# Kernel tuning notes

Hardware: AMD Instinct MI355X
Metric: run time of the kernel (lower is better)

## Reference

```python
import jax, jax.numpy as jnp
import numpy as np

B, IN_SEQ, TGT_SEQ = 128, 50, 25
IN_SIZE, OUT_SIZE, RNN = 128, 128, 2048


def setup_inputs() -> dict:
    key = jax.random.key(0)
    ks = jax.random.split(key, 10)
    s_in = 1.0 / np.sqrt(IN_SIZE)
    s_out = 1.0 / np.sqrt(OUT_SIZE)
    s_rnn = 1.0 / np.sqrt(RNN)
    return {
        "encoder_inputs": jax.random.normal(ks[0], (B, IN_SEQ, IN_SIZE), jnp.float32),
        "decoder_inputs": jax.random.normal(ks[1], (B, TGT_SEQ, IN_SIZE), jnp.float32),
        "fc1_w": jax.random.uniform(ks[2], (OUT_SIZE, IN_SIZE), jnp.float32, -s_in, s_in),
        "fc1_b": jax.random.uniform(ks[3], (OUT_SIZE,), jnp.float32, -s_in, s_in),
        "w_ih": jax.random.uniform(ks[4], (3 * RNN, OUT_SIZE), jnp.float32, -s_rnn, s_rnn),
        "w_hh": jax.random.uniform(ks[5], (3 * RNN, RNN), jnp.float32, -s_rnn, s_rnn),
        "b_ih": jax.random.uniform(ks[6], (3 * RNN,), jnp.float32, -s_rnn, s_rnn),
        "b_hh": jax.random.uniform(ks[7], (3 * RNN,), jnp.float32, -s_rnn, s_rnn),
        "fc2_w": jax.random.uniform(ks[8], (OUT_SIZE, RNN), jnp.float32, -s_rnn, s_rnn),
        "fc2_b": jax.random.uniform(ks[9], (OUT_SIZE,), jnp.float32, -s_rnn, s_rnn),
    }


def _gru_cell(x, h, w_ih, w_hh, b_ih, b_hh):
    # PyTorch GRUCell: gates ordered (r, z, n)
    gi = x @ w_ih.T + b_ih            # [B, 3R]
    gh = h @ w_hh.T + b_hh            # [B, 3R]
    i_r, i_z, i_n = jnp.split(gi, 3, axis=-1)
    h_r, h_z, h_n = jnp.split(gh, 3, axis=-1)
    r = jax.nn.sigmoid(i_r + h_r)
    z = jax.nn.sigmoid(i_z + h_z)
    n = jnp.tanh(i_n + r * h_n)
    return (1.0 - z) * n + z * h


def reference(encoder_inputs, decoder_inputs, fc1_w, fc1_b, w_ih, w_hh, b_ih, b_hh, fc2_w, fc2_b):
    # Eval mode: F.dropout(training=False) is identity.
    enc = encoder_inputs @ fc1_w.T + fc1_b              # [B, S_in, OUT]
    enc_t = jnp.transpose(enc, (1, 0, 2))               # time-major [S_in, B, OUT]
    h0 = jnp.zeros((encoder_inputs.shape[0], RNN), enc.dtype)

    def enc_step(state, x):
        return _gru_cell(x, state, w_ih, w_hh, b_ih, b_hh), None

    state, _ = jax.lax.scan(enc_step, h0, enc_t[:-1])   # input_seq - 1 steps

    def dec_step(carry, _):
        state, inp = carry
        inp = jax.lax.stop_gradient(inp)                # inp.detach()
        state = _gru_cell(inp, state, w_ih, w_hh, b_ih, b_hh)
        out = inp + state @ fc2_w.T + fc2_b             # residual decoder
        return (state, out), out

    _, outs = jax.lax.scan(dec_step, (state, enc_t[-1]), None, length=TGT_SEQ)
    return jnp.transpose(outs, (1, 0, 2))               # [B, TGT_SEQ, OUT]
```

## Files before the change

kernel.cpp:

```cpp
#include <hip/hip_runtime.h>
#include <limits.h>

constexpr int kB   = 128;
constexpr int kSin = 50;
constexpr int kT   = 25;
constexpr int kD   = 128;
constexpr int kR   = 2048;
constexpr int kNB  = 256;
constexpr int kNT  = 512;

typedef __bf16 bf16x8 __attribute__((ext_vector_type(8)));
typedef float  f32x4  __attribute__((ext_vector_type(4)));
typedef unsigned short u16;
typedef unsigned long long u64;

__device__ __forceinline__ float bf2f(u16 u){ union{unsigned i; float f;}x; x.i=((unsigned)u)<<16; return x.f; }
__device__ __forceinline__ u16 f2bf(float f){ union{float f; unsigned i;}x; x.f=f; return (u16)((x.i + 0x7FFFu + ((x.i>>16)&1u))>>16); }
__device__ __forceinline__ float sigm(float x){ return 1.f/(1.f+__expf(-x)); }

__device__ __forceinline__ void stg32(unsigned* p, unsigned v){
    __hip_atomic_store(p, v, __ATOMIC_RELAXED, __HIP_MEMORY_SCOPE_AGENT);
}
__device__ __forceinline__ void stg64(u64* p, u64 v){
    __hip_atomic_store(p, v, __ATOMIC_RELAXED, __HIP_MEMORY_SCOPE_AGENT);
}

__device__ __forceinline__ bf16x8 pack8(float4 a, float4 b){
    union{ bf16x8 v; u16 u[8]; } t;
    t.u[0]=f2bf(a.x); t.u[1]=f2bf(a.y); t.u[2]=f2bf(a.z); t.u[3]=f2bf(a.w);
    t.u[4]=f2bf(b.x); t.u[5]=f2bf(b.y); t.u[6]=f2bf(b.z); t.u[7]=f2bf(b.w);
    return t.v;
}

__device__ __forceinline__ void gbar(int* flags, int* genp, int k)
{
    __syncthreads();
    if (threadIdx.x == 0) atomicMax(&flags[blockIdx.x], k);
    if (blockIdx.x == 0 && threadIdx.x < 64) {
        const int i0 = (int)threadIdx.x * 4;
        for (;;) {
            int a = atomicMax(&flags[i0+0], INT_MIN);
            int b = atomicMax(&flags[i0+1], INT_MIN);
            int c = atomicMax(&flags[i0+2], INT_MIN);
            int d = atomicMax(&flags[i0+3], INT_MIN);
            if (__ballot((a>=k)&&(b>=k)&&(c>=k)&&(d>=k)) == ~0ull) break;
            __builtin_amdgcn_s_sleep(2);
        }
        if (threadIdx.x == 0) atomicMax(genp, k);
    }
    if (threadIdx.x == 0) {
        while (atomicMax(genp, INT_MIN) < k) __builtin_amdgcn_s_sleep(2);
        __builtin_amdgcn_fence(__ATOMIC_ACQUIRE, "agent");
    }
    __syncthreads();
}

__device__ __forceinline__ void cvt_f32_bf16(const float* __restrict__ s, u16* __restrict__ d,
                                             int n4, int gtid, int gstride)
{
    for (int i = gtid; i < n4; i += gstride) {
        float4 v = ((const float4*)s)[i];
        u64 pk = (u64)f2bf(v.x) | ((u64)f2bf(v.y)<<16) | ((u64)f2bf(v.z)<<32) | ((u64)f2bf(v.w)<<48);
        stg64((u64*)d + i, pk);
    }
}

template<int NT, int NACC>
__device__ __forceinline__ void small_gemm(
    const u16* __restrict__ Am, int alda,
    const u16* __restrict__ Bp, int bldb,
    f32x4 (&acc)[NACC], u16* pool)
{
    const int tid=threadIdx.x, lane=tid&63, wv=tid>>6, g=wv>>2, mt=wv&3, ar=lane&15, aq=lane>>4;
    u16* sA = pool;
    u16* sB = pool + 8704;
    { int q=tid,     r=q>>4, c=q&15; *(uint4*)&sA[r*136+c*8] = *(const uint4*)(Am + r*alda + c*8); }
    { int q=tid+512, r=q>>4, c=q&15; *(uint4*)&sA[r*136+c*8] = *(const uint4*)(Am + r*alda + c*8); }
    for (int q=tid; q<NT*256; q+=kNT){
        int r=q>>4, c=q&15;
        *(uint4*)&sB[r*136+c*8] = *(const uint4*)(Bp + (size_t)r*bldb + c*8);
    }
    __syncthreads();
#pragma unroll
    for (int jt=0; jt<NT; ++jt){
        if ((jt&1) != g) continue;
#pragma unroll
        for (int kk=0; kk<4; ++kk){
            bf16x8 a = *(const bf16x8*)&sA[(mt*16+ar)*136 + kk*32 + aq*8];
            bf16x8 b = *(const bf16x8*)&sB[(jt*16+ar)*136 + kk*32 + aq*8];
            acc[jt>>1] = __builtin_amdgcn_mfma_f32_16x16x32_bf16(a,b,acc[jt>>1],0,0,0);
        }
    }
    __syncthreads();
}

__device__ __forceinline__ void gru_phase_reg(
    const u16* __restrict__ hcur, u16* __restrict__ hnxt,
    const u16* __restrict__ xb,
    const bf16x8 (&wB)[3][8], const bf16x8 (&wI)[3],
    const float* __restrict__ bias,
    int wgc, int mrow0, u16* smem)
{
    const int tid=threadIdx.x, lane=tid&63, w=tid>>6, ar=lane&15, aq=lane>>4;
    const f32x4 zz = {0.f,0.f,0.f,0.f};
    f32x4 acc[3][4] = {{zz,zz,zz,zz},{zz,zz,zz,zz},{zz,zz,zz,zz}};
    f32x4 xn[4] = {zz,zz,zz,zz};

#pragma unroll
    for (int mt=0; mt<4; ++mt){
        const int row = mrow0 + mt*16 + ar;
        bf16x8 af[8];
#pragma unroll
        for (int c=0; c<8; ++c){
            const int s = 16*w + 2*c + (aq>>1);
            af[c] = *(const bf16x8*)(hcur + (((s*128 + row)<<4) + (aq&1)*8));
        }
#pragma unroll
        for (int c=0; c<8; ++c){
            acc[0][mt] = __builtin_amdgcn_mfma_f32_16x16x32_bf16(af[c], wB[0][c], acc[0][mt],0,0,0);
            acc[1][mt] = __builtin_amdgcn_mfma_f32_16x16x32_bf16(af[c], wB[1][c], acc[1][mt],0,0,0);
            acc[2][mt] = __builtin_amdgcn_mfma_f32_16x16x32_bf16(af[c], wB[2][c], acc[2][mt],0,0,0);
        }
    }
    if (w < 4){
#pragma unroll
        for (int mt=0; mt<4; ++mt){
            bf16x8 ax = *(const bf16x8*)(xb + (mrow0+mt*16+ar)*kD + 32*w + aq*8);
            acc[0][mt] = __builtin_amdgcn_mfma_f32_16x16x32_bf16(ax, wI[0], acc[0][mt],0,0,0);
            acc[1][mt] = __builtin_amdgcn_mfma_f32_16x16x32_bf16(ax, wI[1], acc[1][mt],0,0,0);
            xn[mt]     = __builtin_amdgcn_mfma_f32_16x16x32_bf16(ax, wI[2], xn[mt],0,0,0);
        }
    }
    float* red = (float*)smem;
#define RCELL(wp,g4,mt) (red + (((((wp)*4+(g4))*4+(mt))*64 + lane)<<2))
    if (w >= 4){
#pragma unroll
        for (int g=0; g<3; ++g)
#pragma unroll
            for (int mt=0; mt<4; ++mt)
                *(f32x4*)RCELL(w-4, g, mt) = acc[g][mt];
    }
    __syncthreads();
    if (w < 4){
#pragma unroll
        for (int g=0; g<3; ++g)
#pragma unroll
            for (int mt=0; mt<4; ++mt)
                acc[g][mt] += *(f32x4*)RCELL(w, g, mt);
#pragma unroll
        for (int g=0; g<3; ++g)
#pragma unroll
            for (int mt=0; mt<4; ++mt)
                *(f32x4*)RCELL(w, g, mt) = acc[g][mt];
#pragma unroll
        for (int mt=0; mt<4; ++mt)
            *(f32x4*)RCELL(w, 3, mt) = xn[mt];
    }
    __syncthreads();
    if (tid < 256){
        const int mt = tid>>6, ls = tid&63, aqs = ls>>4, ars = ls&15;
        f32x4 R=zz, Z=zz, NH=zz, NX=zz;
#pragma unroll
        for (int wp=0; wp<4; ++wp){
            R  += *(f32x4*)(red + ((((wp*4+0)*4+mt)*64 + ls)<<2));
            Z  += *(f32x4*)(red + ((((wp*4+1)*4+mt)*64 + ls)<<2));
            NH += *(f32x4*)(red + ((((wp*4+2)*4+mt)*64 + ls)<<2));
            NX += *(f32x4*)(red + ((((wp*4+3)*4+mt)*64 + ls)<<2));
        }
        const int hc = wgc*16 + ars;
        const float brz = bias[hc]      + bias[3*kR+hc];
        const float bzz = bias[kR+hc]   + bias[4*kR+hc];
        const float bin = bias[2*kR+hc];
        const float bhn = bias[5*kR+hc];
#pragma unroll
        for (int rr=0; rr<4; ++rr){
            const int m = mrow0 + mt*16 + aqs*4 + rr;
            float r_ = sigm(R[rr] + brz);
            float z_ = sigm(Z[rr] + bzz);
            float n_ = tanhf(NX[rr] + bin + r_*(NH[rr] + bhn));
            float hp = bf2f(hcur[((wgc*128 + m)<<4) + ars]);
            u16 hb = f2bf((1.f-z_)*n_ + z_*hp);
            unsigned other = (unsigned)__shfl_xor((int)(unsigned)hb, 1);
            if (!(ars&1))
                stg32((unsigned*)(hnxt + ((wgc*128+m)<<4) + ars), (unsigned)hb | (other<<16));
        }
    }
#undef RCELL
    __syncthreads();
}

__device__ __forceinline__ void fc2_gemm(
    const u16* __restrict__ hnew, const u16* __restrict__ WF2,
    int mrow0, int nt, int ks, float* __restrict__ part_tile, u16* smem)
{
    const int tid=threadIdx.x, lane=tid&63, wv=tid>>6, ar=lane&15, aq=lane>>4;
    u16* sA = smem;
    u16* sB = smem + 8704;
#pragma unroll
    for (int rep=0; rep<2; ++rep){
        int q = tid + rep*512, r = q>>4, c = q&15;
        int s = ks*8 + (c>>1), off = (c&1)*8;
        *(uint4*)&sA[r*136+c*8] = *(const uint4*)(hnew + (((s*128 + mrow0 + r)<<4) + off));
    }
    if (tid < 256){
        int r = tid>>4, c = tid&15;
        *(uint4*)&sB[r*136+c*8] = *(const uint4*)(WF2 + (size_t)(nt*16+r)*kR + ks*128 + c*8);
    }
    __syncthreads();
    if (wv < 4){
        const int mt = wv;
        f32x4 ao = {0.f,0.f,0.f,0.f};
#pragma unroll
        for (int kk=0; kk<4; ++kk){
            bf16x8 a = *(const bf16x8*)&sA[(mt*16+ar)*136 + kk*32 + aq*8];
            bf16x8 b = *(const bf16x8*)&sB[ar*136 + kk*32 + aq*8];
            ao = __builtin_amdgcn_mfma_f32_16x16x32_bf16(a,b,ao,0,0,0);
        }
#pragma unroll
        for (int rr=0; rr<4; ++rr)
            stg32((unsigned*)(part_tile + (mt*16 + aq*4 + rr)*16 + ar), __float_as_uint(ao[rr]));
    }
    __syncthreads();
}

__global__ __launch_bounds__(kNT, 2) void seq2seq_kernel(
    const void* __restrict__ enc_in_raw, const void* __restrict__ fc1_w_raw,
    const void* __restrict__ fc1_b_raw,  const void* __restrict__ w_ih_raw,
    const void* __restrict__ w_hh_raw,   const void* __restrict__ b_ih_raw,
    const void* __restrict__ b_hh_raw,   const void* __restrict__ fc2_w_raw,
    const void* __restrict__ fc2_b_raw,
    void* __restrict__ out_raw,
    u16* __restrict__ enc_act,
    u16* __restrict__ h_b16,
    u16* __restrict__ inp_b16,
    float* __restrict__ inp_f32,
    float* __restrict__ encF,
    float* __restrict__ bias,
    float* __restrict__ part,
    int* flags, int* genp,
    u16* __restrict__ cv_encx, u16* __restrict__ cv_fc2, u16* __restrict__ cv_fc1)
{
    __shared__ __align__(16) u16 smem[32768];
    __shared__ int sflag;
    const int wg = blockIdx.x, tid = threadIdx.x;
    const int wgc = wg & 127, mrow0 = (wg >> 7) * 64;
    const int lane = tid & 63, wv = tid >> 6, ar = lane & 15, aq = lane >> 4;
    const int gtid = wg * kNT + tid, gstride = kNB * kNT;
    int tok = 1;

    {
        const u16* p = (const u16*)enc_in_raw;
        int found = 0;
        for (int i = tid; i < 16384; i += kNT) found |= ((p[i] & 0x7F80) == 0x7F80) ? 1 : 0;
        if (tid == 0) sflag = 0;
        __syncthreads();
        if (found) sflag = 1;
        __syncthreads();
    }
    const bool F32 = (sflag != 0);

    bf16x8 wB[3][8];
    bf16x8 wI[3];
    {
        const int w4 = wv & 3;
        if (F32){
            const float* Wh = (const float*)w_hh_raw;
            const float* Wi = (const float*)w_ih_raw;
#pragma unroll
            for (int g=0; g<3; ++g)
#pragma unroll
                for (int c=0; c<8; ++c){
                    size_t o = (size_t)(g*kR + wgc*16 + ar)*kR + 256*wv + 32*c + aq*8;
                    wB[g][c] = pack8(*(const float4*)(Wh+o), *(const float4*)(Wh+o+4));
                }
#pragma unroll
            for (int g=0; g<3; ++g){
                size_t o = (size_t)(g*kR + wgc*16 + ar)*kD + 32*w4 + aq*8;
                wI[g] = pack8(*(const float4*)(Wi+o), *(const float4*)(Wi+o+4));
            }
        } else {
            const u16* Wh = (const u16*)w_hh_raw;
            const u16* Wi = (const u16*)w_ih_raw;
#pragma unroll
            for (int g=0; g<3; ++g)
#pragma unroll
                for (int c=0; c<8; ++c)
                    wB[g][c] = *(const bf16x8*)(Wh + (size_t)(g*kR + wgc*16 + ar)*kR + 256*wv + 32*c + aq*8);
#pragma unroll
            for (int g=0; g<3; ++g)
                wI[g] = *(const bf16x8*)(Wi + (size_t)(g*kR + wgc*16 + ar)*kD + 32*w4 + aq*8);
        }
    }

    if (F32) {
        cvt_f32_bf16((const float*)fc2_w_raw, cv_fc2,  (kD*kR)/4,       gtid, gstride);
        cvt_f32_bf16((const float*)fc1_w_raw, cv_fc1,  (kD*kD)/4,       gtid, gstride);
        cvt_f32_bf16((const float*)enc_in_raw,cv_encx, (kB*kSin*kD)/4,  gtid, gstride);
        for (int i = gtid; i < 3*kR; i += gstride) {
            stg32((unsigned*)&bias[i],        __float_as_uint(((const float*)b_ih_raw)[i]));
            stg32((unsigned*)&bias[3*kR + i], __float_as_uint(((const float*)b_hh_raw)[i]));
        }
        for (int i = gtid; i < kD; i += gstride) {
            stg32((unsigned*)&bias[6*kR + i],      __float_as_uint(((const float*)fc1_b_raw)[i]));
            stg32((unsigned*)&bias[6*kR + kD + i], __float_as_uint(((const float*)fc2_b_raw)[i]));
        }
    } else {
        for (int i = gtid; i < 3*kR; i += gstride) {
            stg32((unsigned*)&bias[i],        __float_as_uint(bf2f(((const u16*)b_ih_raw)[i])));
            stg32((unsigned*)&bias[3*kR + i], __float_as_uint(bf2f(((const u16*)b_hh_raw)[i])));
        }
        for (int i = gtid; i < kD; i += gstride) {
            stg32((unsigned*)&bias[6*kR + i],      __float_as_uint(bf2f(((const u16*)fc1_b_raw)[i])));
            stg32((unsigned*)&bias[6*kR + kD + i], __float_as_uint(bf2f(((const u16*)fc2_b_raw)[i])));
        }
    }
    for (int i = gtid; i < (kB*kR)/2; i += gstride) stg32((unsigned*)h_b16 + i, 0u);
    gbar(flags, genp, tok++);

    const u16* ENCX = F32 ? cv_encx : (const u16*)enc_in_raw;
    const u16* WF2  = F32 ? cv_fc2  : (const u16*)fc2_w_raw;
    const u16* WF1  = F32 ? cv_fc1  : (const u16*)fc1_w_raw;

    if (wgc < kSin) {
        const int g = wv>>2, mt = wv&3;
        const f32x4 zz = {0.f,0.f,0.f,0.f};
        f32x4 ae[4] = {zz,zz,zz,zz};
        small_gemm<8,4>(ENCX + ((size_t)mrow0*kSin + wgc)*kD, kSin*kD, WF1, kD, ae, smem);
#pragma unroll
        for (int jt=0; jt<8; ++jt){
            if ((jt&1) != g) continue;
            int col = jt*16 + ar;
            float fb = bias[6*kR + col];
#pragma unroll
            for (int rr=0; rr<4; ++rr){
                int m = mrow0 + mt*16 + aq*4 + rr;
                float v = ae[jt>>1][rr] + fb;
                u16 hb = f2bf(v);
                unsigned other = (unsigned)__shfl_xor((int)(unsigned)hb, 1);
                if (!(ar&1))
                    stg32((unsigned*)(enc_act + ((size_t)wgc*kB + m)*kD + col),
                          (unsigned)hb | (other<<16));
                if (wgc == kSin-1)
                    stg32((unsigned*)(encF + (size_t)m*kD + col), __float_as_uint(v));
            }
        }
    }
    gbar(flags, genp, tok++);

    int par = 0;
    for (int t = 0; t < kSin-1; ++t) {
        gru_phase_reg(h_b16 + (size_t)par*kB*kR, h_b16 + (size_t)(1-par)*kB*kR,
                      enc_act + (size_t)t*kB*kD, wB, wI, bias, wgc, mrow0, smem);
        gbar(flags, genp, tok++);
        par ^= 1;
    }

    const u16*   ib  = enc_act + (size_t)(kSin-1)*kB*kD;
    const float* ifp = encF;
    for (int d = 0; d < kT; ++d) {
        gru_phase_reg(h_b16 + (size_t)par*kB*kR, h_b16 + (size_t)(1-par)*kB*kR,
                      ib, wB, wI, bias, wgc, mrow0, smem);
        gbar(flags, genp, tok++);
        par ^= 1;
        const u16* hnew = h_b16 + (size_t)par*kB*kR;

        {
            const int nt = wgc >> 4, ks = wgc & 15;
            float* pt = part + (size_t)((((wg>>7)*8 + nt)*16) + ks) * 1024;
            fc2_gemm(hnew, WF2, mrow0, nt, ks, pt, smem);
        }
        gbar(flags, genp, tok++);

        u16*   nib = inp_b16 + (size_t)(d&1)*kB*kD;
        float* nif = inp_f32 + (size_t)(d&1)*kB*kD;
        if (wgc < 8) {
            const int nt = wgc;
            const float* pt = part + (size_t)(((wg>>7)*8 + nt)*16) * 1024;
            const int e0 = tid*2;
            const int Lm = e0>>4, c0 = e0&15;
            const int m = mrow0 + Lm, col = nt*16 + c0;
            float s0 = 0.f, s1 = 0.f;
#pragma unroll
            for (int ks=0; ks<16; ++ks){ s0 += pt[ks*1024 + e0]; s1 += pt[ks*1024 + e0 + 1]; }
            float o0 = s0 + bias[6*kR + kD + col]     + ifp[(size_t)m*kD + col];
            float o1 = s1 + bias[6*kR + kD + col + 1] + ifp[(size_t)m*kD + col + 1];
            size_t ob = ((size_t)m*kT + d)*kD + col;
            if (F32) { ((float*)out_raw)[ob] = o0; ((float*)out_raw)[ob+1] = o1; }
            else     { ((u16*)out_raw)[ob] = f2bf(o0); ((u16*)out_raw)[ob+1] = f2bf(o1); }
            stg32((unsigned*)(nif + (size_t)m*kD + col),     __float_as_uint(o0));
            stg32((unsigned*)(nif + (size_t)m*kD + col + 1), __float_as_uint(o1));
            stg32((unsigned*)(nib + (size_t)m*kD + col),
                  (unsigned)f2bf(o0) | ((unsigned)f2bf(o1)<<16));
        }
        gbar(flags, genp, tok++);
        ib = nib; ifp = nif;
    }
}

extern "C" void kernel_launch(void* const* d_in, const int* in_sizes, int n_in,
                              void* d_out, int out_size, void* d_ws, size_t ws_size,
                              hipStream_t stream)
{
    size_t off = 0;
    char* ws = (char*)d_ws;
    auto alloc = [&](size_t bytes) -> char* {
        char* p = ws + off;
        off = (off + bytes + 255) & ~(size_t)255;
        return p;
    };
    u16*   enc_act = (u16*)alloc((size_t)kSin*kB*kD*2);
    u16*   h_b16   = (u16*)alloc((size_t)2*kB*kR*2);
    u16*   inp_b16 = (u16*)alloc((size_t)2*kB*kD*2);
    float* inp_f32 = (float*)alloc((size_t)2*kB*kD*4);
    float* encF    = (float*)alloc((size_t)kB*kD*4);
    float* bias    = (float*)alloc((size_t)(6*kR + 2*kD)*4);
    float* part    = (float*)alloc((size_t)256*1024*4);
    int*   flags   = (int*)alloc(kNB*sizeof(int));
    int*   genp    = (int*)alloc(256);
    u16*   cv_encx = (u16*)alloc((size_t)kB*kSin*kD*2);
    u16*   cv_fc2  = (u16*)alloc((size_t)kD*kR*2);
    u16*   cv_fc1  = (u16*)alloc((size_t)kD*kD*2);
    (void)ws_size; (void)in_sizes; (void)n_in; (void)out_size;

    seq2seq_kernel<<<dim3(kNB), dim3(kNT), 0, stream>>>(
        d_in[0], d_in[2], d_in[3], d_in[4], d_in[5], d_in[6], d_in[7], d_in[8], d_in[9],
        d_out,
        enc_act, h_b16, inp_b16, inp_f32, encF, bias, part, flags, genp,
        cv_encx, cv_fc2, cv_fc1);
}
```

Measured before the change: 1.740 ms.

## Fuse fc2 partials into GRU phase and pad/spread barrier flags

After: 1.643 ms. -5.6%, faster.

```diff
diff --git a/kernel.cpp b/kernel.cpp
--- a/kernel.cpp
+++ b/kernel.cpp
@@ -35,21 +35,23 @@
 __device__ __forceinline__ void gbar(int* flags, int* genp, int k)
 {
     __syncthreads();
-    if (threadIdx.x == 0) atomicMax(&flags[blockIdx.x], k);
-    if (blockIdx.x == 0 && threadIdx.x < 64) {
-        const int i0 = (int)threadIdx.x * 4;
+    const int tid = threadIdx.x, wg = blockIdx.x;
+    if (tid == 0) atomicMax(&flags[wg*16], k);
+    if (wg == 0 && tid < 64) {
+        const int i0 = tid * 4;
         for (;;) {
-            int a = atomicMax(&flags[i0+0], INT_MIN);
-            int b = atomicMax(&flags[i0+1], INT_MIN);
-            int c = atomicMax(&flags[i0+2], INT_MIN);
-            int d = atomicMax(&flags[i0+3], INT_MIN);
+            int a = atomicMax(&flags[(i0+0)*16], INT_MIN);
+            int b = atomicMax(&flags[(i0+1)*16], INT_MIN);
+            int c = atomicMax(&flags[(i0+2)*16], INT_MIN);
+            int d = atomicMax(&flags[(i0+3)*16], INT_MIN);
             if (__ballot((a>=k)&&(b>=k)&&(c>=k)&&(d>=k)) == ~0ull) break;
-            __builtin_amdgcn_s_sleep(2);
-        }
-        if (threadIdx.x == 0) atomicMax(genp, k);
-    }
-    if (threadIdx.x == 0) {
-        while (atomicMax(genp, INT_MIN) < k) __builtin_amdgcn_s_sleep(2);
+            __builtin_amdgcn_s_sleep(1);
+        }
+        atomicMax(&genp[tid*16], k);
+    }
+    if (tid == 0) {
+        if (wg != 0)
+            while (atomicMax(&genp[(wg&63)*16], INT_MIN) < k) __builtin_amdgcn_s_sleep(1);
         __builtin_amdgcn_fence(__ATOMIC_ACQUIRE, "agent");
     }
     __syncthreads();
@@ -98,8 +100,8 @@
     const u16* __restrict__ hcur, u16* __restrict__ hnxt,
     const u16* __restrict__ xb,
     const bf16x8 (&wB)[3][8], const bf16x8 (&wI)[3],
-    const float* __restrict__ bias,
-    int wgc, int mrow0, u16* smem)
+    const float4 b4, float (&hprev)[4],
+    int wgc, int mrow0, u16* smem, u16* sH)
 {
     const int tid=threadIdx.x, lane=tid&63, w=tid>>6, ar=lane&15, aq=lane>>4;
     const f32x4 zz = {0.f,0.f,0.f,0.f};
@@ -167,19 +169,16 @@
             NH += *(f32x4*)(red + ((((wp*4+2)*4+mt)*64 + ls)<<2));
             NX += *(f32x4*)(red + ((((wp*4+3)*4+mt)*64 + ls)<<2));
         }
-        const int hc = wgc*16 + ars;
-        const float brz = bias[hc]      + bias[3*kR+hc];
-        const float bzz = bias[kR+hc]   + bias[4*kR+hc];
-        const float bin = bias[2*kR+hc];
-        const float bhn = bias[5*kR+hc];
 #pragma unroll
         for (int rr=0; rr<4; ++rr){
             const int m = mrow0 + mt*16 + aqs*4 + rr;
-            float r_ = sigm(R[rr] + brz);
-            float z_ = sigm(Z[rr] + bzz);
-            float n_ = tanhf(NX[rr] + bin + r_*(NH[rr] + bhn));
-            float hp = bf2f(hcur[((wgc*128 + m)<<4) + ars]);
-            u16 hb = f2bf((1.f-z_)*n_ + z_*hp);
+            float r_ = sigm(R[rr] + b4.x);
+            float z_ = sigm(Z[rr] + b4.y);
+            float n_ = tanhf(NX[rr] + b4.z + r_*(NH[rr] + b4.w));
+            float hn = (1.f-z_)*n_ + z_*hprev[rr];
+            hprev[rr] = hn;
+            u16 hb = f2bf(hn);
+            sH[(mt*16 + aqs*4 + rr)*16 + ars] = hb;
             unsigned other = (unsigned)__shfl_xor((int)(unsigned)hb, 1);
             if (!(ars&1))
                 stg32((unsigned*)(hnxt + ((wgc*128+m)<<4) + ars), (unsigned)hb | (other<<16));
@@ -189,38 +188,33 @@
     __syncthreads();
 }
 
-__device__ __forceinline__ void fc2_gemm(
-    const u16* __restrict__ hnew, const u16* __restrict__ WF2,
-    int mrow0, int nt, int ks, float* __restrict__ part_tile, u16* smem)
-{
-    const int tid=threadIdx.x, lane=tid&63, wv=tid>>6, ar=lane&15, aq=lane>>4;
-    u16* sA = smem;
-    u16* sB = smem + 8704;
-#pragma unroll
-    for (int rep=0; rep<2; ++rep){
-        int q = tid + rep*512, r = q>>4, c = q&15;
-        int s = ks*8 + (c>>1), off = (c&1)*8;
-        *(uint4*)&sA[r*136+c*8] = *(const uint4*)(hnew + (((s*128 + mrow0 + r)<<4) + off));
-    }
-    if (tid < 256){
-        int r = tid>>4, c = tid&15;
-        *(uint4*)&sB[r*136+c*8] = *(const uint4*)(WF2 + (size_t)(nt*16+r)*kR + ks*128 + c*8);
-    }
-    __syncthreads();
-    if (wv < 4){
-        const int mt = wv;
-        f32x4 ao = {0.f,0.f,0.f,0.f};
-#pragma unroll
-        for (int kk=0; kk<4; ++kk){
-            bf16x8 a = *(const bf16x8*)&sA[(mt*16+ar)*136 + kk*32 + aq*8];
-            bf16x8 b = *(const bf16x8*)&sB[ar*136 + kk*32 + aq*8];
-            ao = __builtin_amdgcn_mfma_f32_16x16x32_bf16(a,b,ao,0,0,0);
-        }
-#pragma unroll
-        for (int rr=0; rr<4; ++rr)
-            stg32((unsigned*)(part_tile + (mt*16 + aq*4 + rr)*16 + ar), __float_as_uint(ao[rr]));
-    }
-    __syncthreads();
+__device__ __forceinline__ void fc2_partial(
+    const u16* __restrict__ sH, const bf16x8 (&wF2)[4],
+    int wgc, int mh, float* __restrict__ part)
+{
+    const int tid=threadIdx.x, lane=tid&63, w=tid>>6, ar=lane&15, aq=lane>>4;
+    const int mt = w&3, nh = w>>2;
+    bf16x8 a;
+    if (aq < 2) a = *(const bf16x8*)&sH[(mt*16+ar)*16 + aq*8];
+    else {
+#pragma unroll
+        for (int i=0;i<8;++i) a[i] = (__bf16)0.f;
+    }
+    const f32x4 zz = {0.f,0.f,0.f,0.f};
+    f32x4 acc[4] = {zz,zz,zz,zz};
+#pragma unroll
+    for (int j=0;j<4;++j)
+        acc[j] = __builtin_amdgcn_mfma_f32_16x16x32_bf16(a, wF2[j], acc[j],0,0,0);
+#pragma unroll
+    for (int j=0;j<4;++j){
+        const int col = (nh*4+j)*16 + ar;
+#pragma unroll
+        for (int rr=0;rr<4;++rr){
+            const int row = mt*16 + aq*4 + rr;
+            stg32((unsigned*)(part + ((((size_t)mh*64+row)*128 + wgc)*128 + col)),
+                  __float_as_uint(acc[j][rr]));
+        }
+    }
 }
 
 __global__ __launch_bounds__(kNT, 2) void seq2seq_kernel(
@@ -240,8 +234,9 @@
     int* flags, int* genp,
     u16* __restrict__ cv_encx, u16* __restrict__ cv_fc2, u16* __restrict__ cv_fc1)
 {
-    __shared__ __align__(16) u16 smem[32768];
+    __shared__ __align__(16) u16 smem[33792];
     __shared__ int sflag;
+    u16* sH = smem + 32768;
     const int wg = blockIdx.x, tid = threadIdx.x;
     const int wgc = wg & 127, mrow0 = (wg >> 7) * 64;
     const int lane = tid & 63, wv = tid >> 6, ar = lane & 15, aq = lane >> 4;
@@ -320,6 +315,30 @@
     const u16* ENCX = F32 ? cv_encx : (const u16*)enc_in_raw;
     const u16* WF2  = F32 ? cv_fc2  : (const u16*)fc2_w_raw;
     const u16* WF1  = F32 ? cv_fc1  : (const u16*)fc1_w_raw;
+
+    float4 b4;
+    {
+        const int hc = wgc*16 + ar;
+        b4.x = bias[hc]      + bias[3*kR+hc];
+        b4.y = bias[kR+hc]   + bias[4*kR+hc];
+        b4.z = bias[2*kR+hc];
+        b4.w = bias[5*kR+hc];
+    }
+    bf16x8 wF2[4];
+    {
+        const int nh = wv>>2;
+#pragma unroll
+        for (int j=0;j<4;++j){
+            if (aq < 2)
+                wF2[j] = *(const bf16x8*)(WF2 + (size_t)((nh*4+j)*16+ar)*kR + wgc*16 + aq*8);
+            else {
+#pragma unroll
+                for (int i=0;i<8;++i) wF2[j][i] = (__bf16)0.f;
+            }
+        }
+    }
+    const float fc2b = bias[6*kR + kD + (wg&1)*64 + (tid&63)];
+    float hprev[4] = {0.f, 0.f, 0.f, 0.f};
 
     if (wgc < kSin) {
         const int g = wv>>2, mt = wv&3;
@@ -350,47 +369,49 @@
     int par = 0;
     for (int t = 0; t < kSin-1; ++t) {
         gru_phase_reg(h_b16 + (size_t)par*kB*kR, h_b16 + (size_t)(1-par)*kB*kR,
-                      enc_act + (size_t)t*kB*kD, wB, wI, bias, wgc, mrow0, smem);
+                      enc_act + (size_t)t*kB*kD, wB, wI, b4, hprev, wgc, mrow0, smem, sH);
         gbar(flags, genp, tok++);
         par ^= 1;
     }
 
     const u16*   ib  = enc_act + (size_t)(kSin-1)*kB*kD;
     const float* ifp = encF;
+    const int mh = wg >> 7;
     for (int d = 0; d < kT; ++d) {
         gru_phase_reg(h_b16 + (size_t)par*kB*kR, h_b16 + (size_t)(1-par)*kB*kR,
-                      ib, wB, wI, bias, wgc, mrow0, smem);
+                      ib, wB, wI, b4, hprev, wgc, mrow0, smem, sH);
+        fc2_partial(sH, wF2, wgc, mh, part);
         gbar(flags, genp, tok++);
         par ^= 1;
-        const u16* hnew = h_b16 + (size_t)par*kB*kR;
-
-        {
-            const int nt = wgc >> 4, ks = wgc & 15;
-            float* pt = part + (size_t)((((wg>>7)*8 + nt)*16) + ks) * 1024;
-            fc2_gemm(hnew, WF2, mrow0, nt, ks, pt, smem);
-        }
-        gbar(flags, genp, tok++);
 
         u16*   nib = inp_b16 + (size_t)(d&1)*kB*kD;
         float* nif = inp_f32 + (size_t)(d&1)*kB*kD;
-        if (wgc < 8) {
-            const int nt = wgc;
-            const float* pt = part + (size_t)(((wg>>7)*8 + nt)*16) * 1024;
-            const int e0 = tid*2;
-            const int Lm = e0>>4, c0 = e0&15;
-            const int m = mrow0 + Lm, col = nt*16 + c0;
-            float s0 = 0.f, s1 = 0.f;
-#pragma unroll
-            for (int ks=0; ks<16; ++ks){ s0 += pt[ks*1024 + e0]; s1 += pt[ks*1024 + e0 + 1]; }
-            float o0 = s0 + bias[6*kR + kD + col]     + ifp[(size_t)m*kD + col];
-            float o1 = s1 + bias[6*kR + kD + col + 1] + ifp[(size_t)m*kD + col + 1];
-            size_t ob = ((size_t)m*kT + d)*kD + col;
-            if (F32) { ((float*)out_raw)[ob] = o0; ((float*)out_raw)[ob+1] = o1; }
-            else     { ((u16*)out_raw)[ob] = f2bf(o0); ((u16*)out_raw)[ob+1] = f2bf(o1); }
-            stg32((unsigned*)(nif + (size_t)m*kD + col),     __float_as_uint(o0));
-            stg32((unsigned*)(nif + (size_t)m*kD + col + 1), __float_as_uint(o1));
-            stg32((unsigned*)(nib + (size_t)m*kD + col),
-                  (unsigned)f2bf(o0) | ((unsigned)f2bf(o1)<<16));
+        {
+            const int row = wg >> 1, ch = wg & 1;
+            const int mh2 = row >> 6, rl = row & 63;
+            const float* pr = part + (size_t)((mh2*64 + rl)*128)*128;
+            const int cl = tid & 63, sg = tid >> 6;
+            float s = 0.f;
+#pragma unroll
+            for (int j=0;j<16;++j) s += pr[(size_t)(sg*16+j)*128 + ch*64 + cl];
+            float* red2 = (float*)smem;
+            red2[sg*64 + cl] = s;
+            __syncthreads();
+            if (tid < 64){
+                float t2 = 0.f;
+#pragma unroll
+                for (int g2=0; g2<8; ++g2) t2 += red2[g2*64 + tid];
+                const int colg = ch*64 + tid;
+                const float o = t2 + fc2b + ifp[(size_t)row*kD + colg];
+                const size_t ob = ((size_t)row*kT + d)*kD + colg;
+                if (F32) ((float*)out_raw)[ob] = o;
+                else     ((u16*)out_raw)[ob]   = f2bf(o);
+                stg32((unsigned*)(nif + (size_t)row*kD + colg), __float_as_uint(o));
+                u16 hb = f2bf(o);
+                unsigned other = (unsigned)__shfl_xor((int)(unsigned)hb, 1);
+                if (!(tid&1))
+                    stg32((unsigned*)(nib + (size_t)row*kD + colg), (unsigned)hb | (other<<16));
+            }
         }
         gbar(flags, genp, tok++);
         ib = nib; ifp = nif;
@@ -414,9 +435,9 @@
     float* inp_f32 = (float*)alloc((size_t)2*kB*kD*4);
     float* encF    = (float*)alloc((size_t)kB*kD*4);
     float* bias    = (float*)alloc((size_t)(6*kR + 2*kD)*4);
-    float* part    = (float*)alloc((size_t)256*1024*4);
-    int*   flags   = (int*)alloc(kNB*sizeof(int));
-    int*   genp    = (int*)alloc(256);
+    float* part    = (float*)alloc((size_t)2*64*128*128*4);
+    int*   flags   = (int*)alloc((size_t)kNB*16*4);
+    int*   genp    = (int*)alloc((size_t)64*16*4);
     u16*   cv_encx = (u16*)alloc((size_t)kB*kSin*kD*2);
     u16*   cv_fc2  = (u16*)alloc((size_t)kD*kR*2);
     u16*   cv_fc1  = (u16*)alloc((size_t)kD*kD*2);
```
